# Kernel optimization log

Hardware: AMD Instinct MI355X
Metric: run time of the kernel (lower is better)

Reference implementation:

```python
import jax, jax.numpy as jnp
import numpy as np

B, T, C, HS = 8, 4096, 1024, 64  # batch, seq, n_embd, head_size


def setup_inputs() -> dict:
    key = jax.random.key(0)
    kx, kk, kq, kv = jax.random.split(key, 4)
    x = jax.random.normal(kx, (B, T, C), dtype=jnp.float32)
    # bias-free linear weights, stored as [in, out] like flax kernels
    s = 1.0 / np.sqrt(C)
    Wk = jax.random.normal(kk, (C, HS), dtype=jnp.float32) * s
    Wq = jax.random.normal(kq, (C, HS), dtype=jnp.float32) * s
    Wv = jax.random.normal(kv, (C, HS), dtype=jnp.float32) * s
    return {"x": x, "Wk": Wk, "Wq": Wq, "Wv": Wv}


def reference(x, Wk, Wq, Wv):
    # x: [B, T, C]
    Tq = x.shape[1]
    Cdim = x.shape[2]
    k = jnp.einsum('btc,ch->bth', x, Wk)  # [B,T,HS]
    q = jnp.einsum('btc,ch->bth', x, Wq)
    v = jnp.einsum('btc,ch->bth', x, Wv)
    # NOTE: original scales by C**-0.5 (full embed dim), not head_size**-0.5
    scale = Cdim ** (-0.5)
    wei = jnp.einsum('bth,bsh->bts', q, k) * scale  # [B,T,T]
    causal = jnp.tril(jnp.ones((Tq, Tq), dtype=bool))
    wei = jnp.where(causal, wei, -jnp.inf)
    wei = jax.nn.softmax(wei, axis=-1)
    out = jnp.einsum('bts,bsh->bth', wei, v)  # [B,T,HS]
    return out
```

## Files before the change

### kernel.cpp

```cpp
#include <hip/hip_runtime.h>
#include <hip/hip_bf16.h>


typedef __attribute__((ext_vector_type(8))) short short8;
typedef __attribute__((ext_vector_type(4))) float f32x4;
typedef __attribute__((ext_vector_type(16))) float f32x16;
typedef __attribute__((ext_vector_type(4))) unsigned int u32x4;

#define NB 8
#define NT 4096
#define NC 1024
#define NH 64

__device__ __forceinline__ unsigned short f2bf(float f) {
    unsigned int u = __builtin_bit_cast(unsigned int, f);
    u += 0x7fffu + ((u >> 16) & 1u);
    return (unsigned short)(u >> 16);
}

__device__ __forceinline__ unsigned cvt_pk_bf16(float lo, float hi) {
    unsigned r;
    asm("v_cvt_pk_bf16_f32 %0, %1, %2" : "=v"(r) : "v"(lo), "v"(hi));
    return r;
}

#define GLOAD16(gp, lp)                                                        \
    __builtin_amdgcn_global_load_lds(                                          \
        (const __attribute__((address_space(1))) void*)(gp),                   \
        (__attribute__((address_space(3))) void*)(lp), 16, 0, 0)

__global__ __launch_bounds__(256) void wprep_kernel(
    const float* __restrict__ Wk, const float* __restrict__ Wq,
    const float* __restrict__ Wv, unsigned short* __restrict__ Wt)
{
    int n = blockIdx.x;
    int which = n >> 6, h = n & 63;
    const float* W = (which == 0) ? Wk : (which == 1) ? Wq : Wv;
    for (int c = threadIdx.x; c < NC; c += 256)
        Wt[(size_t)n * NC + c] = f2bf(W[(size_t)c * NH + h]);
}

__global__ __launch_bounds__(256, 2) void proj_kernel(
    const float* __restrict__ x, const unsigned short* __restrict__ Wt,
    unsigned short* __restrict__ qws, unsigned short* __restrict__ kws,
    unsigned short* __restrict__ vtws)
{
    __shared__ char lds[4][20480];

    const int lane = threadIdx.x & 63;
    const int wave = threadIdx.x >> 6;
    const int l15 = lane & 15;
    const int kg = lane >> 4;
    const int m0 = blockIdx.x * 64;

    const int agS = (lane & 7) ^ (lane >> 3);
    const float* aSrc[2];
#pragma unroll
    for (int j = 0; j < 2; ++j) {
        int i = wave * 2 + j;
        int r = 8 * i + (lane >> 3);
        aSrc[j] = x + (size_t)(m0 + r) * NC + agS * 4;
    }
    const int bgS = (lane & 3) ^ ((lane >> 2) & 3);
    const unsigned short* bSrc[3];
#pragma unroll
    for (int j = 0; j < 3; ++j) {
        int u = wave * 3 + j;
        int r = 16 * u + (lane >> 2);
        bSrc[j] = Wt + (size_t)r * NC + bgS * 8;
    }

    f32x4 acc[12];
#pragma unroll
    for (int i = 0; i < 12; ++i) acc[i] = f32x4{0.f, 0.f, 0.f, 0.f};

#define STAGE_CHUNK(c)                                                         \
    do {                                                                       \
        char* base_ = lds[(c) & 3];                                            \
        _Pragma("unroll")                                                      \
        for (int j = 0; j < 2; ++j)                                            \
            GLOAD16(aSrc[j] + (c) * 32, base_ + (wave * 2 + j) * 1024);        \
        _Pragma("unroll")                                                      \
        for (int j = 0; j < 3; ++j)                                            \
            GLOAD16(bSrc[j] + (c) * 32, base_ + 8192 + (wave * 3 + j) * 1024); \
    } while (0)

    STAGE_CHUNK(0);
    STAGE_CHUNK(1);

    for (int kc = 0; kc < 32; ++kc) {
        if (kc < 30) {
            STAGE_CHUNK(kc + 2);
            asm volatile("s_waitcnt vmcnt(10)" ::: "memory");
        } else if (kc == 30) {
            asm volatile("s_waitcnt vmcnt(5)" ::: "memory");
        } else {
            asm volatile("s_waitcnt vmcnt(0)" ::: "memory");
        }
        __builtin_amdgcn_sched_barrier(0);
        __builtin_amdgcn_s_barrier();

        const char* Ab = lds[kc & 3];
        const char* Bb = lds[kc & 3] + 8192;
        {
            const int r = wave * 16 + l15;
            const int g0 = kg * 2;
            f32x4 a0 = *(const f32x4*)(Ab + r * 128 + ((g0 ^ (r & 7)) * 16));
            f32x4 a1 = *(const f32x4*)(Ab + r * 128 + (((g0 + 1) ^ (r & 7)) * 16));
            short8 a;
            a[0] = (short)f2bf(a0[0]); a[1] = (short)f2bf(a0[1]);
            a[2] = (short)f2bf(a0[2]); a[3] = (short)f2bf(a0[3]);
            a[4] = (short)f2bf(a1[0]); a[5] = (short)f2bf(a1[1]);
            a[6] = (short)f2bf(a1[2]); a[7] = (short)f2bf(a1[3]);
#pragma unroll
            for (int nt = 0; nt < 12; ++nt) {
                int rb = nt * 16 + l15;
                short8 bfrag = *(const short8*)(
                    Bb + rb * 64 + ((kg ^ (rb & 3)) * 16));
                acc[nt] = __builtin_amdgcn_mfma_f32_16x16x32_bf16(a, bfrag, acc[nt], 0, 0, 0);
            }
        }
    }
#undef STAGE_CHUNK

    const float cs = 0.04508422f;
    const int crow0 = m0 + wave * 16 + (kg << 2);
#pragma unroll
    for (int nt = 0; nt < 12; ++nt) {
        int n = nt * 16 + l15;
        int which = n >> 6;
        int h = n & 63;
#pragma unroll
        for (int r = 0; r < 4; ++r) {
            int gm = crow0 + r;
            float av = acc[nt][r];
            if (which == 1) av *= cs;
            unsigned short v = f2bf(av);
            if (which == 0) {
                kws[(size_t)gm * NH + h] = v;
            } else if (which == 1) {
                qws[(size_t)gm * NH + h] = v;
            } else {
                int bb = gm >> 12, tt = gm & 4095;
                vtws[((size_t)(bb * NH + h)) * NT + tt] = v;
            }
        }
    }
}

__global__ __launch_bounds__(256, 4) void flash_kernel(
    const unsigned short* __restrict__ qws, const unsigned short* __restrict__ kws,
    const unsigned short* __restrict__ vtws,
    float* __restrict__ opart, float* __restrict__ mlpart)
{
    __shared__ unsigned short Kbuf[2][64 * 64];
    __shared__ unsigned short Vbuf[2][64 * 64];

    const int id = blockIdx.x;
    const int g = id >> 5;
    const int p = (id >> 3) & 3;
    const int b = id & 7;
    const int a = g & 7, m = g >> 3;
    const int qt = (m == 0) ? 31 - a : (m == 1) ? 16 + a : (m == 2) ? 15 - a : a;
    const int n = 2 * qt + 2;
    const int len = (n + 3) >> 2;
    const int k0 = p * len;
    const int k1 = (k0 + len < n) ? (k0 + len) : n;
    const int pid = id;

    float* mlp = mlpart + (size_t)pid * 256;
    float* op  = opart + (size_t)pid * 8192;

    const int lane = threadIdx.x & 63;
    const int wave = threadIdx.x >> 6;
    const int l31 = lane & 31;
    const int hi = lane >> 5;
    const int rsw = lane & 7;

    const int sg = (lane & 7) ^ (lane >> 3);
    const unsigned short* kSrc[2];
    const unsigned short* vSrc[2];
#pragma unroll
    for (int j = 0; j < 2; ++j) {
        int r = 16 * wave + 8 * j + (lane >> 3);
        kSrc[j] = kws + ((size_t)(b * NT) + r) * NH + sg * 8;
        vSrc[j] = vtws + ((size_t)(b * NH + r)) * NT + sg * 8;
    }

    const int qmin = qt * 128 + wave * 32;
    short8 qf[4];
    {
        const char* qp = (const char*)(qws + ((size_t)(b * NT) + qmin + l31) * NH);
#pragma unroll
        for (int s = 0; s < 4; ++s)
            qf[s] = *(const short8*)(qp + s * 32 + hi * 16);
    }

    f32x16 o0, o1;
#pragma unroll
    for (int i = 0; i < 16; ++i) { o0[i] = 0.f; o1[i] = 0.f; }
    float m_r = -INFINITY;
    float l_r = 0.f;

    const int kst = (k0 < n) ? k0 : (n - 1);
#pragma unroll
    for (int j = 0; j < 2; ++j) {
        int i = 2 * wave + j;
        GLOAD16(kSrc[j] + (size_t)kst * 64 * NH, (char*)Kbuf[0] + i * 1024);
        GLOAD16(vSrc[j] + (size_t)kst * 64,      (char*)Vbuf[0] + i * 1024);
    }
    __syncthreads();

    int cur = 0;
    for (int kv = k0; kv < k1; ++kv) {
        if (kv + 1 < k1) {
#pragma unroll
            for (int j = 0; j < 2; ++j) {
                int i = 2 * wave + j;
                GLOAD16(kSrc[j] + (size_t)(kv + 1) * 64 * NH,
                        (char*)Kbuf[cur ^ 1] + i * 1024);
                GLOAD16(vSrc[j] + (size_t)(kv + 1) * 64,
                        (char*)Vbuf[cur ^ 1] + i * 1024);
            }
        }

        const char* Kb = (const char*)Kbuf[cur];
        const char* Vb = (const char*)Vbuf[cur];

        f32x16 st0, st1;
#pragma unroll
        for (int i = 0; i < 16; ++i) { st0[i] = 0.f; st1[i] = 0.f; }
        __builtin_amdgcn_s_setprio(1);
#pragma unroll
        for (int s = 0; s < 4; ++s) {
            int gl = s * 2 + hi;
            short8 ka = *(const short8*)(Kb + l31 * 128 + ((gl ^ rsw) << 4));
            short8 kb = *(const short8*)(Kb + (32 + l31) * 128 + ((gl ^ rsw) << 4));
            st0 = __builtin_amdgcn_mfma_f32_32x32x16_bf16(ka, qf[s], st0, 0, 0, 0);
            st1 = __builtin_amdgcn_mfma_f32_32x32x16_bf16(kb, qf[s], st1, 0, 0, 0);
        }
        __builtin_amdgcn_s_setprio(0);

        const int kb0 = kv * 64;
        if (kb0 + 63 > qmin) {
            const int qg = qmin + l31;
#pragma unroll
            for (int r = 0; r < 16; ++r) {
                int key = kb0 + (r & 3) + 8 * (r >> 2) + 4 * hi;
                if (key > qg) st0[r] = -1e30f;
                if (key + 32 > qg) st1[r] = -1e30f;
            }
        }

        float lmax = st0[0];
#pragma unroll
        for (int r = 1; r < 16; ++r) lmax = fmaxf(lmax, st0[r]);
#pragma unroll
        for (int r = 0; r < 16; ++r) lmax = fmaxf(lmax, st1[r]);

        if (!__all(lmax <= m_r + 8.0f)) {
            float pmax = fmaxf(lmax, __shfl_xor(lmax, 32));
            float mn = fmaxf(m_r, pmax);
            float alpha = __builtin_amdgcn_exp2f(m_r - mn);
            m_r = mn;
            l_r *= alpha;
#pragma unroll
            for (int r = 0; r < 16; ++r) { o0[r] *= alpha; o1[r] *= alpha; }
        }

        float psum = 0.f;
#pragma unroll
        for (int r = 0; r < 16; ++r) {
            st0[r] = __builtin_amdgcn_exp2f(st0[r] - m_r);
            st1[r] = __builtin_amdgcn_exp2f(st1[r] - m_r);
            psum += st0[r] + st1[r];
        }
        l_r += psum;

        __builtin_amdgcn_s_setprio(1);
#pragma unroll
        for (int kt = 0; kt < 2; ++kt) {
            const f32x16& st = kt ? st1 : st0;
            unsigned pa0 = cvt_pk_bf16(st[0], st[1]),  pa1 = cvt_pk_bf16(st[2], st[3]);
            unsigned pb0 = cvt_pk_bf16(st[4], st[5]),  pb1 = cvt_pk_bf16(st[6], st[7]);
            unsigned pc0 = cvt_pk_bf16(st[8], st[9]),  pc1 = cvt_pk_bf16(st[10], st[11]);
            unsigned pd0 = cvt_pk_bf16(st[12], st[13]), pd1 = cvt_pk_bf16(st[14], st[15]);
            unsigned xa0 = __shfl_xor((int)pa0, 32), xa1 = __shfl_xor((int)pa1, 32);
            unsigned xb0 = __shfl_xor((int)pb0, 32), xb1 = __shfl_xor((int)pb1, 32);
            unsigned xc0 = __shfl_xor((int)pc0, 32), xc1 = __shfl_xor((int)pc1, 32);
            unsigned xd0 = __shfl_xor((int)pd0, 32), xd1 = __shfl_xor((int)pd1, 32);
            u32x4 wA, wB;
            wA[0] = hi ? xb0 : pa0;  wA[1] = hi ? xb1 : pa1;
            wA[2] = hi ? pb0 : xa0;  wA[3] = hi ? pb1 : xa1;
            wB[0] = hi ? xd0 : pc0;  wB[1] = hi ? xd1 : pc1;
            wB[2] = hi ? pd0 : xc0;  wB[3] = hi ? pd1 : xc1;
            short8 pfA = __builtin_bit_cast(short8, wA);
            short8 pfB = __builtin_bit_cast(short8, wB);
#pragma unroll
            for (int w = 0; w < 2; ++w) {
                short8 pf = w ? pfB : pfA;
                int gv = (kt * 2 + w) * 2 + hi;
                short8 va = *(const short8*)(Vb + l31 * 128 + ((gv ^ rsw) << 4));
                short8 vb = *(const short8*)(Vb + (32 + l31) * 128 + ((gv ^ rsw) << 4));
                o0 = __builtin_amdgcn_mfma_f32_32x32x16_bf16(va, pf, o0, 0, 0, 0);
                o1 = __builtin_amdgcn_mfma_f32_32x32x16_bf16(vb, pf, o1, 0, 0, 0);
            }
        }
        __builtin_amdgcn_s_setprio(0);

        __syncthreads();
        cur ^= 1;
    }

    float lt = l_r + __shfl_xor(l_r, 32);
    const int row = wave * 32 + l31;
    float* orow = op + row * 64;
#pragma unroll
    for (int blk = 0; blk < 4; ++blk) {
        f32x4 v0, v1;
#pragma unroll
        for (int r = 0; r < 4; ++r) { v0[r] = o0[blk * 4 + r]; v1[r] = o1[blk * 4 + r]; }
        *(f32x4*)(orow + 8 * blk + 4 * hi) = v0;
        *(f32x4*)(orow + 32 + 8 * blk + 4 * hi) = v1;
    }
    if (hi == 0) {
        mlp[row] = m_r;
        mlp[128 + row] = lt;
    }
}

__global__ __launch_bounds__(256) void combine_kernel(
    const float* __restrict__ opart, const float* __restrict__ mlpart,
    float* __restrict__ out)
{
    const int cid = blockIdx.x;
    const int qt = cid >> 3, b = cid & 7;
    int g;
    if (qt >= 24) g = 31 - qt;
    else if (qt >= 16) g = 8 + (qt - 16);
    else if (qt >= 8) g = 16 + (15 - qt);
    else g = 24 + qt;
    const int pidb = g * 32 + b;

    const float* ml[4];
    const f32x4* ov[4];
#pragma unroll
    for (int p = 0; p < 4; ++p) {
        ml[p] = mlpart + (size_t)(pidb + p * 8) * 256;
        ov[p] = (const f32x4*)(opart + (size_t)(pidb + p * 8) * 8192);
    }
    f32x4* og = (f32x4*)out;

#pragma unroll
    for (int i = 0; i < 8; ++i) {
        int gidx = threadIdx.x + i * 256;
        int row = gidx >> 4;
        float m0 = ml[0][row], m1 = ml[1][row], m2 = ml[2][row], m3 = ml[3][row];
        float ms = fmaxf(fmaxf(m0, m1), fmaxf(m2, m3));
        float e0 = __builtin_amdgcn_exp2f(m0 - ms);
        float e1 = __builtin_amdgcn_exp2f(m1 - ms);
        float e2 = __builtin_amdgcn_exp2f(m2 - ms);
        float e3 = __builtin_amdgcn_exp2f(m3 - ms);
        float den = e0 * ml[0][128 + row] + e1 * ml[1][128 + row] +
                    e2 * ml[2][128 + row] + e3 * ml[3][128 + row];
        float dinv = __builtin_amdgcn_rcpf(den);
        f32x4 a0 = ov[0][gidx], a1 = ov[1][gidx], a2 = ov[2][gidx], a3 = ov[3][gidx];
        f32x4 r;
#pragma unroll
        for (int c = 0; c < 4; ++c)
            r[c] = (e0 * a0[c] + e1 * a1[c] + e2 * a2[c] + e3 * a3[c]) * dinv;
        og[((size_t)(b * NT) + qt * 128 + row) * 16 + (gidx & 15)] = r;
    }
}

extern "C" void kernel_launch(void* const* d_in, const int* in_sizes, int n_in,
                              void* d_out, int out_size, void* d_ws, size_t ws_size,
                              hipStream_t stream) {
    const float* x  = (const float*)d_in[0];
    const float* Wk = (const float*)d_in[1];
    const float* Wq = (const float*)d_in[2];
    const float* Wv = (const float*)d_in[3];
    float* out = (float*)d_out;

    unsigned short* ws   = (unsigned short*)d_ws;
    const size_t qkv_elems = (size_t)NB * NT * NH;
    unsigned short* qws  = ws;
    unsigned short* kws  = qws + qkv_elems;
    unsigned short* vtws = kws + qkv_elems;
    unsigned short* Wt   = vtws + qkv_elems;
    float* opart  = (float*)(Wt + (size_t)192 * NC);
    float* mlpart = opart + (size_t)1024 * 8192;

    wprep_kernel<<<dim3(192), dim3(256), 0, stream>>>(Wk, Wq, Wv, Wt);
    proj_kernel<<<dim3(512), dim3(256), 0, stream>>>(x, Wt, qws, kws, vtws);
    flash_kernel<<<dim3(1024), dim3(256), 0, stream>>>(qws, kws, vtws, opart, mlpart);
    combine_kernel<<<dim3(256), dim3(256), 0, stream>>>(opart, mlpart, out);
}
```

Baseline: 79.53 us.

## Load K/V fragments directly from global memory instead of LDS double buffer

Removes the shared-memory double-buffered staging of K and V tiles, along with the per-iteration barrier. Each wave now reads its MFMA operand fragments straight from global memory (served by L2/L1). This drops the LDS traffic and synchronisation cost. In exchange, the four waves redundantly fetch the same K/V data and prefetch overlap is lost, leaving load latency exposed on the MFMA path.

```diff
diff --git a/kernel.cpp b/kernel.cpp
--- a/kernel.cpp
+++ b/kernel.cpp
@@ -153,9 +153,6 @@
     const unsigned short* __restrict__ vtws,
     float* __restrict__ opart, float* __restrict__ mlpart)
 {
-    __shared__ unsigned short Kbuf[2][64 * 64];
-    __shared__ unsigned short Vbuf[2][64 * 64];
-
     const int id = blockIdx.x;
     const int g = id >> 5;
     const int p = (id >> 3) & 3;
@@ -166,26 +163,17 @@
     const int len = (n + 3) >> 2;
     const int k0 = p * len;
     const int k1 = (k0 + len < n) ? (k0 + len) : n;
-    const int pid = id;
-
-    float* mlp = mlpart + (size_t)pid * 256;
-    float* op  = opart + (size_t)pid * 8192;
+
+    float* mlp = mlpart + (size_t)id * 256;
+    float* op  = opart + (size_t)id * 8192;
 
     const int lane = threadIdx.x & 63;
     const int wave = threadIdx.x >> 6;
     const int l31 = lane & 31;
     const int hi = lane >> 5;
-    const int rsw = lane & 7;
-
-    const int sg = (lane & 7) ^ (lane >> 3);
-    const unsigned short* kSrc[2];
-    const unsigned short* vSrc[2];
-#pragma unroll
-    for (int j = 0; j < 2; ++j) {
-        int r = 16 * wave + 8 * j + (lane >> 3);
-        kSrc[j] = kws + ((size_t)(b * NT) + r) * NH + sg * 8;
-        vSrc[j] = vtws + ((size_t)(b * NH + r)) * NT + sg * 8;
-    }
+
+    const unsigned short* kRow = kws + ((size_t)(b * NT) + l31) * NH + hi * 8;
+    const unsigned short* vRow = vtws + ((size_t)(b * NH) + l31) * NT + hi * 8;
 
     const int qmin = qt * 128 + wave * 32;
     short8 qf[4];
@@ -202,30 +190,9 @@
     float m_r = -INFINITY;
     float l_r = 0.f;
 
-    const int kst = (k0 < n) ? k0 : (n - 1);
-#pragma unroll
-    for (int j = 0; j < 2; ++j) {
-        int i = 2 * wave + j;
-        GLOAD16(kSrc[j] + (size_t)kst * 64 * NH, (char*)Kbuf[0] + i * 1024);
-        GLOAD16(vSrc[j] + (size_t)kst * 64,      (char*)Vbuf[0] + i * 1024);
-    }
-    __syncthreads();
-
-    int cur = 0;
     for (int kv = k0; kv < k1; ++kv) {
-        if (kv + 1 < k1) {
-#pragma unroll
-            for (int j = 0; j < 2; ++j) {
-                int i = 2 * wave + j;
-                GLOAD16(kSrc[j] + (size_t)(kv + 1) * 64 * NH,
-                        (char*)Kbuf[cur ^ 1] + i * 1024);
-                GLOAD16(vSrc[j] + (size_t)(kv + 1) * 64,
-                        (char*)Vbuf[cur ^ 1] + i * 1024);
-            }
-        }
-
-        const char* Kb = (const char*)Kbuf[cur];
-        const char* Vb = (const char*)Vbuf[cur];
+        const unsigned short* kb_ = kRow + (size_t)kv * 64 * NH;
+        const unsigned short* vb_ = vRow + kv * 64;
 
         f32x16 st0, st1;
 #pragma unroll
@@ -233,11 +200,10 @@
         __builtin_amdgcn_s_setprio(1);
 #pragma unroll
         for (int s = 0; s < 4; ++s) {
-            int gl = s * 2 + hi;
-            short8 ka = *(const short8*)(Kb + l31 * 128 + ((gl ^ rsw) << 4));
-            short8 kb = *(const short8*)(Kb + (32 + l31) * 128 + ((gl ^ rsw) << 4));
+            short8 ka = *(const short8*)(kb_ + s * 16);
+            short8 kc = *(const short8*)(kb_ + 32 * NH + s * 16);
             st0 = __builtin_amdgcn_mfma_f32_32x32x16_bf16(ka, qf[s], st0, 0, 0, 0);
-            st1 = __builtin_amdgcn_mfma_f32_32x32x16_bf16(kb, qf[s], st1, 0, 0, 0);
+            st1 = __builtin_amdgcn_mfma_f32_32x32x16_bf16(kc, qf[s], st1, 0, 0, 0);
         }
         __builtin_amdgcn_s_setprio(0);
 
@@ -299,17 +265,14 @@
 #pragma unroll
             for (int w = 0; w < 2; ++w) {
                 short8 pf = w ? pfB : pfA;
-                int gv = (kt * 2 + w) * 2 + hi;
-                short8 va = *(const short8*)(Vb + l31 * 128 + ((gv ^ rsw) << 4));
-                short8 vb = *(const short8*)(Vb + (32 + l31) * 128 + ((gv ^ rsw) << 4));
+                int koff = (kt * 2 + w) * 16;
+                short8 va = *(const short8*)(vb_ + koff);
+                short8 vb = *(const short8*)(vb_ + 32 * NT + koff);
                 o0 = __builtin_amdgcn_mfma_f32_32x32x16_bf16(va, pf, o0, 0, 0, 0);
                 o1 = __builtin_amdgcn_mfma_f32_32x32x16_bf16(vb, pf, o1, 0, 0, 0);
             }
         }
         __builtin_amdgcn_s_setprio(0);
-
-        __syncthreads();
-        cur ^= 1;
     }
 
     float lt = l_r + __shfl_xor(l_r, 32);
```

After: 115.1 us. 44.8% more time.
